# Kernel tuning notes

Measured on AMD Instinct MI355X. Metric: run time of the kernel, lower is better.

Reference implementation:

```python
import jax, jax.numpy as jnp
import numpy as np

NEG_INF = -1e9  # matches torch masked_fill value of -1000000000.0


def setup_inputs() -> dict:
    key = jax.random.key(0)
    k1, k2, k3, k4 = jax.random.split(key, 4)
    B, H, S, D = 4, 16, 2048, 128
    query = jax.random.normal(k1, (B, H, S, D), dtype=jnp.float32)
    key_t = jax.random.normal(k2, (B, H, S, D), dtype=jnp.float32)
    value = jax.random.normal(k3, (B, H, S, D), dtype=jnp.float32)
    mask = jax.random.randint(k4, (B, 1, 1, S), 0, 2, dtype=jnp.int32)
    return {"query": query, "key": key_t, "value": value, "mask": mask, "dropout": 0}


def reference(query, key, value, mask, dropout):
    # scores = Q K^T / sqrt(d_k)   [B,H,S,S]
    d_k = query.shape[-1]
    scores = jnp.einsum("bhqd,bhkd->bhqk", query, key) / jnp.sqrt(jnp.asarray(d_k, query.dtype))
    # masked_fill_(mask == 0, -1e9); mask broadcasts [B,1,1,S] -> [B,H,S,S]
    scores = jnp.where(mask == 0, jnp.asarray(NEG_INF, scores.dtype), scores)
    # dropout == 0 -> identity (deterministic reference / eval mode)
    attn = jax.nn.softmax(scores, axis=-1)
    return jnp.einsum("bhqk,bhkd->bhqd", attn, value)
```

## Files before the change

### kernel.cpp

```cpp
#include <hip/hip_runtime.h>
#include <hip/hip_bf16.h>

#define S_LEN 2048
#define D_DIM 128
#define QBLK 256
#define KVBLK 32
#define NT (S_LEN / KVBLK)
#define KCHUNK 8192
#define VCHUNK 8192
#define PRE_BYTES ((size_t)64 * NT * (KCHUNK + VCHUNK))

typedef __attribute__((ext_vector_type(8))) short short8v;
typedef __attribute__((ext_vector_type(16))) float f32x16;

static __device__ __forceinline__ unsigned f2bf2(float lo, float hi) {
    float2 f2; f2.x = lo; f2.y = hi;
    __hip_bfloat162 h2 = __float22bfloat162_rn(f2);
    unsigned r;
    __builtin_memcpy(&r, &h2, 4);
    return r;
}

static __device__ __forceinline__ void plswap(unsigned& a, unsigned& b) {
    auto r = __builtin_amdgcn_permlane32_swap(a, b, false, false);
    a = r[0]; b = r[1];
}
static __device__ __forceinline__ float plswap_sum(float x) {
    unsigned a = __float_as_uint(x), b = a;
    plswap(a, b);
    return __uint_as_float(a) + __uint_as_float(b);
}

static __device__ __forceinline__ void gload16(const void* g, void* l) {
    __builtin_amdgcn_global_load_lds(
        (const __attribute__((address_space(1))) unsigned int*)g,
        (__attribute__((address_space(3))) unsigned int*)l,
        16, 0, 0);
}

static __device__ __forceinline__ void stage8k(const unsigned char* g, unsigned char* l,
                                               int wv, int lane) {
#pragma unroll
    for (int i = 0; i < 2; ++i) {
        const int off = (wv * 2 + i) * 1024;
        gload16(g + off + lane * 16, l + off);
    }
}

#define VTS 133

__global__ __launch_bounds__(256) void preconv(
    const float* __restrict__ Kp, const float* __restrict__ Vp,
    unsigned short* __restrict__ Ko, unsigned short* __restrict__ Vo)
{
    __shared__ float vt[64 * VTS];
    const int tid = threadIdx.x;
    const int blk = blockIdx.x;
    const size_t gbase = (size_t)(blk >> 5) * S_LEN * D_DIM + (size_t)(blk & 31) * 64 * D_DIM;

#pragma unroll
    for (int i = 0; i < 8; ++i) {
        int idx = (tid + 256 * i) * 4;
        int row = idx >> 7, col = idx & 127;
        float4 v4 = *(const float4*)(Vp + gbase + idx);
        float* d = &vt[row * VTS + col];
        d[0] = v4.x; d[1] = v4.y; d[2] = v4.z; d[3] = v4.w;
    }

    unsigned short* kout = Ko + (size_t)blk * 8192;
#pragma unroll
    for (int i = 0; i < 4; ++i) {
        int o = tid + 256 * i;
        int row = o >> 4, bs = o & 15;
        int b = (bs & 8) | ((bs ^ row) & 7);
        const float* gp = Kp + gbase + row * D_DIM + 8 * b;
        float4 x = *(const float4*)gp;
        float4 y = *(const float4*)(gp + 4);
        uint4 w;
        w.x = f2bf2(x.x, x.y); w.y = f2bf2(x.z, x.w);
        w.z = f2bf2(y.x, y.y); w.w = f2bf2(y.z, y.w);
        *(uint4*)(kout + o * 8) = w;
    }
    __syncthreads();

    unsigned short* vout = Vo + (size_t)blk * 8192;
#pragma unroll
    for (int i = 0; i < 4; ++i) {
        int u = tid + 256 * i;
        int ch = u >> 9, r = u & 511;
        int d = r >> 2, bs = r & 3;
        int b = bs ^ ((d >> 1) & 3);
        const float* c0 = &vt[(ch * 32 + 8 * b) * VTS + d];
        uint4 w;
        w.x = f2bf2(c0[0 * VTS], c0[1 * VTS]);
        w.y = f2bf2(c0[2 * VTS], c0[3 * VTS]);
        w.z = f2bf2(c0[4 * VTS], c0[5 * VTS]);
        w.w = f2bf2(c0[6 * VTS], c0[7 * VTS]);
        *(uint4*)(vout + u * 8) = w;
    }
}

#define ASMEM (16384 + 16384 + 8192)

__global__ __launch_bounds__(256, 2) void sdpa_fwd_pre(
    const float* __restrict__ Qp, const unsigned short* __restrict__ Kpre,
    const unsigned short* __restrict__ Vpre, const int* __restrict__ Mp,
    float* __restrict__ Op)
{
    extern __shared__ unsigned char smem[];
    unsigned char* KbB = smem;
    unsigned char* VbB = smem + 16384;
    float* blds = (float*)(smem + 32768);

    const int tid  = threadIdx.x;
    const int lane = tid & 63;
    const int wv   = tid >> 6;
    const int h    = lane >> 5;
    const int c31  = lane & 31;
    const int hrx  = h ^ (c31 & 7);
    const int vsx  = (c31 >> 1) & 3;
    const int lbid = ((blockIdx.x & 7) << 6) | (blockIdx.x >> 3);
    const int bh   = lbid >> 3;
    const int q0   = (lbid & 7) * QBLK;
    const int bb   = bh >> 4;
    const size_t base = (size_t)bh * S_LEN * D_DIM;
    const unsigned char* Kg = (const unsigned char*)Kpre + (size_t)bh * (NT * KCHUNK);
    const unsigned char* Vg = (const unsigned char*)Vpre + (size_t)bh * (NT * VCHUNK);

    constexpr float SC   = 0.08838834764831845f * 1.4426950408889634f;
    constexpr float NEGB = -1.4426950408889634e9f;
    constexpr float M2   = 16.0f;

    {
        const int* mp = Mp + bb * S_LEN;
#pragma unroll
        for (int i = 0; i < S_LEN / 256; ++i)
            blds[tid + 256 * i] = mp[tid + 256 * i] ? -M2 : NEGB;
    }

    short8v qf0[8], qf1[8];
#pragma unroll
    for (int g = 0; g < 2; ++g) {
        const float* qrp = Qp + base + (size_t)(q0 + 64 * wv + 32 * g + c31) * D_DIM;
#pragma unroll
        for (int kk = 0; kk < 8; ++kk) {
            float4 x = *(const float4*)(qrp + 16 * kk + 8 * h);
            float4 y = *(const float4*)(qrp + 16 * kk + 8 * h + 4);
            uint4 w;
            w.x = f2bf2(x.x * SC, x.y * SC); w.y = f2bf2(x.z * SC, x.w * SC);
            w.z = f2bf2(y.x * SC, y.y * SC); w.w = f2bf2(y.z * SC, y.w * SC);
            if (g == 0) *(uint4*)&qf0[kk] = w; else *(uint4*)&qf1[kk] = w;
        }
    }

    stage8k(Kg, KbB, wv, lane);
    stage8k(Vg, VbB, wv, lane);
    __syncthreads();

    f32x16 acc0[4], acc1[4];
#pragma unroll
    for (int dt = 0; dt < 4; ++dt)
#pragma unroll
        for (int i = 0; i < 16; ++i) { acc0[dt][i] = 0.f; acc1[dt][i] = 0.f; }

    float lp0 = 0.f, lp1 = 0.f;
    int cur = 0;

#pragma unroll 1
    for (int t0 = 0; t0 < NT; ++t0) {
        const unsigned char* KcB = KbB + cur * KCHUNK;
        const unsigned char* VcB = VbB + cur * VCHUNK;

        if (t0 + 1 < NT) {
            stage8k(Kg + (size_t)(t0 + 1) * KCHUNK, KbB + (cur ^ 1) * KCHUNK, wv, lane);
            stage8k(Vg + (size_t)(t0 + 1) * VCHUNK, VbB + (cur ^ 1) * VCHUNK, wv, lane);
        }

        f32x16 s0, s1;
        {
            const float* bp = blds + t0 * KVBLK + 4 * h;
#pragma unroll
            for (int t4 = 0; t4 < 4; ++t4) {
                float4 b4 = *(const float4*)(bp + 8 * t4);
                s0[4 * t4 + 0] = b4.x; s0[4 * t4 + 1] = b4.y;
                s0[4 * t4 + 2] = b4.z; s0[4 * t4 + 3] = b4.w;
                s1[4 * t4 + 0] = b4.x; s1[4 * t4 + 1] = b4.y;
                s1[4 * t4 + 2] = b4.z; s1[4 * t4 + 3] = b4.w;
            }
        }

        __builtin_amdgcn_s_setprio(1);
        {
            const unsigned char* rowp = KcB + (c31 << 8);
#pragma unroll
            for (int kk = 0; kk < 8; ++kk) {
                const int bs = ((2 * kk) & 8) | (((2 * kk) & 7) ^ hrx);
                short8v kf = *(const short8v*)(rowp + (bs << 4));
                s0 = __builtin_amdgcn_mfma_f32_32x32x16_bf16(kf, qf0[kk], s0, 0, 0, 0);
                s1 = __builtin_amdgcn_mfma_f32_32x32x16_bf16(kf, qf1[kk], s1, 0, 0, 0);
            }
        }
        __builtin_amdgcn_s_setprio(0);

        unsigned w00[4], w10[4], w01[4], w11[4];
#pragma unroll
        for (int t4 = 0; t4 < 4; ++t4) {
            float e0 = __builtin_amdgcn_exp2f(s0[4 * t4 + 0]);
            float e1 = __builtin_amdgcn_exp2f(s0[4 * t4 + 1]);
            float e2 = __builtin_amdgcn_exp2f(s0[4 * t4 + 2]);
            float e3 = __builtin_amdgcn_exp2f(s0[4 * t4 + 3]);
            w00[t4] = f2bf2(e0, e1);
            w10[t4] = f2bf2(e2, e3);
            lp0 += (e0 + e1) + (e2 + e3);
            float f0 = __builtin_amdgcn_exp2f(s1[4 * t4 + 0]);
            float f1 = __builtin_amdgcn_exp2f(s1[4 * t4 + 1]);
            float f2 = __builtin_amdgcn_exp2f(s1[4 * t4 + 2]);
            float f3 = __builtin_amdgcn_exp2f(s1[4 * t4 + 3]);
            w01[t4] = f2bf2(f0, f1);
            w11[t4] = f2bf2(f2, f3);
            lp1 += (f0 + f1) + (f2 + f3);
        }

        __builtin_amdgcn_s_setprio(1);
#pragma unroll
        for (int kk = 0; kk < 2; ++kk) {
            unsigned ax0 = w00[2 * kk], bx0 = w00[2 * kk + 1];
            plswap(ax0, bx0);
            unsigned ay0 = w10[2 * kk], by0 = w10[2 * kk + 1];
            plswap(ay0, by0);
            uint4 pw0; pw0.x = ax0; pw0.y = ay0; pw0.z = bx0; pw0.w = by0;
            short8v pf0 = *(short8v*)&pw0;
            unsigned ax1 = w01[2 * kk], bx1 = w01[2 * kk + 1];
            plswap(ax1, bx1);
            unsigned ay1 = w11[2 * kk], by1 = w11[2 * kk + 1];
            plswap(ay1, by1);
            uint4 pw1; pw1.x = ax1; pw1.y = ay1; pw1.z = bx1; pw1.w = by1;
            short8v pf1 = *(short8v*)&pw1;
            const int bs = (2 * kk + h) ^ vsx;
#pragma unroll
            for (int dt = 0; dt < 4; ++dt) {
                short8v vf = *(const short8v*)(VcB + ((32 * dt + c31) << 6) + (bs << 4));
                acc0[dt] = __builtin_amdgcn_mfma_f32_32x32x16_bf16(vf, pf0, acc0[dt], 0, 0, 0);
                acc1[dt] = __builtin_amdgcn_mfma_f32_32x32x16_bf16(vf, pf1, acc1[dt], 0, 0, 0);
            }
        }
        __builtin_amdgcn_s_setprio(0);

        __syncthreads();
        cur ^= 1;
    }

    const float linv0 = 1.0f / plswap_sum(lp0);
    const float linv1 = 1.0f / plswap_sum(lp1);
    float* sw = (float*)(smem + wv * (32 * 68 * 4));
#define EPILOG(ACC, LINV, G)                                                     \
    {                                                                            \
        _Pragma("unroll")                                                        \
        for (int ph = 0; ph < 2; ++ph) {                                         \
            _Pragma("unroll")                                                    \
            for (int dp = 0; dp < 2; ++dp) {                                     \
                const int dtg = 2 * ph + dp;                                     \
                _Pragma("unroll")                                                \
                for (int r = 0; r < 16; ++r) {                                   \
                    int dloc = 32 * dp + (r & 3) + 8 * (r >> 2) + 4 * h;         \
                    sw[c31 * 68 + dloc] = ACC[dtg][r] * (LINV);                  \
                }                                                                \
            }                                                                    \
            _Pragma("unroll")                                                    \
            for (int it = 0; it < 8; ++it) {                                     \
                int f4 = lane + 64 * it;                                         \
                int qq = f4 >> 4, c4 = f4 & 15;                                  \
                float4 val = *(const float4*)&sw[qq * 68 + 4 * c4];              \
                *(float4*)(Op + base + (size_t)(q0 + 64 * wv + 32 * (G) + qq)    \
                           * D_DIM + 64 * ph + 4 * c4) = val;                    \
            }                                                                    \
        }                                                                        \
    }
    EPILOG(acc0, linv0, 0)
    EPILOG(acc1, linv1, 1)
#undef EPILOG
}

#define FBKV 64
#define FBNT (S_LEN / FBKV)
#define FBQB 128
#define KSTRIDE 136
#define VSTRIDE 72
#define KELEMS (FBKV * KSTRIDE)
#define VELEMS (D_DIM * VSTRIDE)
#define KBYTES (2 * KELEMS * 2)
#define VBYTES (2 * VELEMS * 2)
#define FBSMEM (KBYTES + VBYTES + S_LEN * 4)

struct KReg { float4 a[4][2]; };
struct VReg { float4 a[2][4]; };

static __device__ __forceinline__ void load_K(KReg& kr, const float* Kbase,
                                              int kv0, int kr0, int kc8) {
#pragma unroll
    for (int i = 0; i < 4; ++i) {
        const float* gp = Kbase + (size_t)(kv0 + kr0 + 16 * i) * D_DIM + 8 * kc8;
        kr.a[i][0] = *(const float4*)gp;
        kr.a[i][1] = *(const float4*)(gp + 4);
    }
}
static __device__ __forceinline__ void write_K(const KReg& kr, unsigned short* Kn,
                                               int kr0, int kc8) {
#pragma unroll
    for (int i = 0; i < 4; ++i) {
        uint4 w;
        w.x = f2bf2(kr.a[i][0].x, kr.a[i][0].y);
        w.y = f2bf2(kr.a[i][0].z, kr.a[i][0].w);
        w.z = f2bf2(kr.a[i][1].x, kr.a[i][1].y);
        w.w = f2bf2(kr.a[i][1].z, kr.a[i][1].w);
        *(uint4*)&Kn[(kr0 + 16 * i) * KSTRIDE + 8 * kc8] = w;
    }
}
static __device__ __forceinline__ void load_V(VReg& vr, const float* Vbase,
                                              int kv0, int vkq, int vdg) {
#pragma unroll
    for (int ii = 0; ii < 2; ++ii)
#pragma unroll
        for (int r = 0; r < 4; ++r)
            vr.a[ii][r] = *(const float4*)(Vbase + (size_t)(kv0 + 4 * vkq + 32 * ii + r) * D_DIM + 4 * vdg);
}
static __device__ __forceinline__ void write_V(const VReg& vr, unsigned short* Vn,
                                               int vkq, int vdg) {
#pragma unroll
    for (int ii = 0; ii < 2; ++ii) {
        const int kvb = 4 * vkq + 32 * ii;
        const int d0  = 4 * vdg;
        uint2 u;
        u.x = f2bf2(vr.a[ii][0].x, vr.a[ii][1].x); u.y = f2bf2(vr.a[ii][2].x, vr.a[ii][3].x);
        *(uint2*)&Vn[(d0 + 0) * VSTRIDE + kvb] = u;
        u.x = f2bf2(vr.a[ii][0].y, vr.a[ii][1].y); u.y = f2bf2(vr.a[ii][2].y, vr.a[ii][3].y);
        *(uint2*)&Vn[(d0 + 1) * VSTRIDE + kvb] = u;
        u.x = f2bf2(vr.a[ii][0].z, vr.a[ii][1].z); u.y = f2bf2(vr.a[ii][2].z, vr.a[ii][3].z);
        *(uint2*)&Vn[(d0 + 2) * VSTRIDE + kvb] = u;
        u.x = f2bf2(vr.a[ii][0].w, vr.a[ii][1].w); u.y = f2bf2(vr.a[ii][2].w, vr.a[ii][3].w);
        *(uint2*)&Vn[(d0 + 3) * VSTRIDE + kvb] = u;
    }
}

__global__ __launch_bounds__(256, 2) void sdpa_fwd_fb(
    const float* __restrict__ Qp, const float* __restrict__ Kp,
    const float* __restrict__ Vp, const int* __restrict__ Mp,
    float* __restrict__ Op)
{
    extern __shared__ unsigned char smem[];
    unsigned short* Kb   = (unsigned short*)smem;
    unsigned short* Vb   = (unsigned short*)(smem + KBYTES);
    float*          mlds = (float*)(smem + KBYTES + VBYTES);

    const int tid  = threadIdx.x;
    const int lane = tid & 63;
    const int wv   = tid >> 6;
    const int h    = lane >> 5;
    const int c31  = lane & 31;
    const int bid  = blockIdx.x;
    const int bh   = bid >> 4;
    const int q0   = (bid & 15) * FBQB;
    const int bb   = bh >> 4;
    const size_t base = (size_t)bh * S_LEN * D_DIM;

    constexpr float SC   = 0.08838834764831845f * 1.4426950408889634f;
    constexpr float NEGB = -1.4426950408889634e9f;
    constexpr float THR  = 11.541560327111708f;

    {
        const int* mp = Mp + bb * S_LEN;
#pragma unroll
        for (int i = 0; i < S_LEN / 256; ++i)
            mlds[tid + 256 * i] = mp[tid + 256 * i] ? 0.f : NEGB;
    }

    short8v qf[8];
    {
        const float* qrp = Qp + base + (size_t)(q0 + 32 * wv + c31) * D_DIM;
#pragma unroll
        for (int kk = 0; kk < 8; ++kk) {
            float4 x = *(const float4*)(qrp + 16 * kk + 8 * h);
            float4 y = *(const float4*)(qrp + 16 * kk + 8 * h + 4);
            uint4 w;
            w.x = f2bf2(x.x, x.y); w.y = f2bf2(x.z, x.w);
            w.z = f2bf2(y.x, y.y); w.w = f2bf2(y.z, y.w);
            *(uint4*)&qf[kk] = w;
        }
    }

    const int kc8 = tid & 15;
    const int kr0 = tid >> 4;
    const int vdg = tid & 31;
    const int vkq = tid >> 5;

    {
        KReg kr; VReg vr;
        load_K(kr, Kp + base, 0, kr0, kc8);
        load_V(vr, Vp + base, 0, vkq, vdg);
        write_K(kr, Kb, kr0, kc8);
        write_V(vr, Vb, vkq, vdg);
    }
    __syncthreads();

    f32x16 acc[4];
#pragma unroll
    for (int dt = 0; dt < 4; ++dt)
#pragma unroll
        for (int i = 0; i < 16; ++i) acc[dt][i] = 0.f;

    float m2 = -INFINITY;
    float lsum = 0.f;
    int cur = 0;

#pragma unroll 1
    for (int t0 = 0; t0 < FBNT; ++t0) {
        const int kv0 = t0 * FBKV;
        unsigned short* Kc = Kb + cur * KELEMS;
        unsigned short* Vc = Vb + cur * VELEMS;
        unsigned short* Kn = Kb + (cur ^ 1) * KELEMS;
        unsigned short* Vn = Vb + (cur ^ 1) * VELEMS;
        const bool pf = (t0 + 1 < FBNT);

        KReg kr; VReg vr;
        if (pf) {
            load_K(kr, Kp + base, kv0 + FBKV, kr0, kc8);
            load_V(vr, Vp + base, kv0 + FBKV, vkq, vdg);
        }

        f32x16 stc[2];
        __builtin_amdgcn_s_setprio(1);
#pragma unroll
        for (int c = 0; c < 2; ++c) {
            f32x16 s;
#pragma unroll
            for (int i = 0; i < 16; ++i) s[i] = 0.f;
#pragma unroll
            for (int kk = 0; kk < 8; ++kk) {
                short8v kf = *(const short8v*)&Kc[(32 * c + c31) * KSTRIDE + 16 * kk + 8 * h];
                s = __builtin_amdgcn_mfma_f32_32x32x16_bf16(kf, qf[kk], s, 0, 0, 0);
            }
            stc[c] = s;
        }
        __builtin_amdgcn_s_setprio(0);

        float p[2][16];
#pragma unroll
        for (int c = 0; c < 2; ++c)
#pragma unroll
            for (int t = 0; t < 4; ++t) {
                float4 b4 = *(const float4*)&mlds[kv0 + 32 * c + 8 * t + 4 * h];
                p[c][4 * t + 0] = fmaf(stc[c][4 * t + 0], SC, b4.x);
                p[c][4 * t + 1] = fmaf(stc[c][4 * t + 1], SC, b4.y);
                p[c][4 * t + 2] = fmaf(stc[c][4 * t + 2], SC, b4.z);
                p[c][4 * t + 3] = fmaf(stc[c][4 * t + 3], SC, b4.w);
            }

        float pmax = -INFINITY;
#pragma unroll
        for (int c = 0; c < 2; ++c)
#pragma unroll
            for (int r = 0; r < 16; ++r) pmax = fmaxf(pmax, p[c][r]);
        pmax = fmaxf(pmax, __shfl_xor(pmax, 32));
        if (!__all(pmax <= m2 + THR)) {
            float mnew = fmaxf(m2, pmax);
            float fr = __builtin_amdgcn_exp2f(m2 - mnew);
            m2 = mnew;
            lsum *= fr;
#pragma unroll
            for (int dt = 0; dt < 4; ++dt)
#pragma unroll
                for (int i = 0; i < 16; ++i) acc[dt][i] *= fr;
        }
        float ssum = 0.f;
#pragma unroll
        for (int c = 0; c < 2; ++c)
#pragma unroll
            for (int r = 0; r < 16; ++r) {
                float e = __builtin_amdgcn_exp2f(p[c][r] - m2);
                p[c][r] = e; ssum += e;
            }
        ssum += __shfl_xor(ssum, 32);
        lsum += ssum;

        unsigned w0[2][4], w1[2][4];
#pragma unroll
        for (int c = 0; c < 2; ++c)
#pragma unroll
            for (int t = 0; t < 4; ++t) {
                w0[c][t] = f2bf2(p[c][4 * t + 0], p[c][4 * t + 1]);
                w1[c][t] = f2bf2(p[c][4 * t + 2], p[c][4 * t + 3]);
            }

        __builtin_amdgcn_s_setprio(1);
#pragma unroll
        for (int kk = 0; kk < 4; ++kk) {
            const int t0i = (2 * kk) & 3,     c0i = (2 * kk) >> 2;
            const int t1i = (2 * kk + 1) & 3, c1i = (2 * kk + 1) >> 2;
            unsigned own0 = h ? w0[c1i][t1i] : w0[c0i][t0i];
            unsigned own1 = h ? w1[c1i][t1i] : w1[c0i][t0i];
            unsigned snd0 = h ? w0[c0i][t0i] : w0[c1i][t1i];
            unsigned snd1 = h ? w1[c0i][t0i] : w1[c1i][t1i];
            unsigned r0 = __shfl_xor(snd0, 32);
            unsigned r1 = __shfl_xor(snd1, 32);
            uint4 pw;
            pw.x = h ? r0 : own0;  pw.y = h ? r1 : own1;
            pw.z = h ? own0 : r0;  pw.w = h ? own1 : r1;
            short8v pfv = *(short8v*)&pw;
#pragma unroll
            for (int dt = 0; dt < 4; ++dt) {
                short8v vf = *(const short8v*)&Vc[(32 * dt + c31) * VSTRIDE + 16 * kk + 8 * h];
                acc[dt] = __builtin_amdgcn_mfma_f32_32x32x16_bf16(vf, pfv, acc[dt], 0, 0, 0);
            }
        }
        __builtin_amdgcn_s_setprio(0);

        if (pf) {
            write_K(kr, Kn, kr0, kc8);
            write_V(vr, Vn, vkq, vdg);
        }
        __syncthreads();
        cur ^= 1;
    }

    __syncthreads();
    const float linv = 1.0f / lsum;
    float* sw = (float*)(smem + wv * (32 * 68 * 4));
#pragma unroll
    for (int ph = 0; ph < 2; ++ph) {
#pragma unroll
        for (int dp = 0; dp < 2; ++dp) {
            const int dtg = 2 * ph + dp;
#pragma unroll
            for (int r = 0; r < 16; ++r) {
                int dloc = 32 * dp + (r & 3) + 8 * (r >> 2) + 4 * h;
                sw[c31 * 68 + dloc] = acc[dtg][r] * linv;
            }
        }
#pragma unroll
        for (int it = 0; it < 8; ++it) {
            int f4 = lane + 64 * it;
            int qq = f4 >> 4, c4 = f4 & 15;
            float4 val = *(const float4*)&sw[qq * 68 + 4 * c4];
            *(float4*)(Op + base + (size_t)(q0 + 32 * wv + qq) * D_DIM + 64 * ph + 4 * c4) = val;
        }
    }
}

extern "C" void kernel_launch(void* const* d_in, const int* in_sizes, int n_in,
                              void* d_out, int out_size, void* d_ws, size_t ws_size,
                              hipStream_t stream) {
    (void)in_sizes; (void)n_in; (void)out_size;
    const float* Q = (const float*)d_in[0];
    const float* K = (const float*)d_in[1];
    const float* V = (const float*)d_in[2];
    const int*   M = (const int*)d_in[3];
    float*       O = (float*)d_out;

    if (ws_size >= PRE_BYTES) {
        unsigned short* Kpre = (unsigned short*)d_ws;
        unsigned short* Vpre = (unsigned short*)((char*)d_ws + PRE_BYTES / 2);
        hipLaunchKernelGGL(preconv, dim3(64 * 32), dim3(256), 0, stream, K, V, Kpre, Vpre);
        hipLaunchKernelGGL(sdpa_fwd_pre, dim3(64 * (S_LEN / QBLK)), dim3(256), ASMEM, stream,
                           Q, Kpre, Vpre, M, O);
    } else {
        hipLaunchKernelGGL(sdpa_fwd_fb, dim3(1024), dim3(256), FBSMEM, stream, Q, K, V, M, O);
    }
}
```

Baseline: 201.6 us.

## Software-pipeline QK^T one tile ahead of softmax and PV

Restructures the main loop so the QK^T MFMA for tile t+1 is issued after the PV MFMAs of tile t, with K staged two tiles ahead and V one tile ahead. A prologue computes the first score tile before the loop. This is meant to let the exp and convert work overlap with independent MFMA chains and to hide the LDS latency of K fragments. In exchange it adds a live score register set across iterations, which may raise register pressure, and it changes the buffer indexing.

```diff
diff --git a/kernel.cpp b/kernel.cpp
--- a/kernel.cpp
+++ b/kernel.cpp
@@ -155,6 +155,7 @@
 
     stage8k(Kg, KbB, wv, lane);
     stage8k(Vg, VbB, wv, lane);
+    stage8k(Kg + KCHUNK, KbB + KCHUNK, wv, lane);
     __syncthreads();
 
     f32x16 acc0[4], acc1[4];
@@ -162,45 +163,37 @@
     for (int dt = 0; dt < 4; ++dt)
 #pragma unroll
         for (int i = 0; i < 16; ++i) { acc0[dt][i] = 0.f; acc1[dt][i] = 0.f; }
-
     float lp0 = 0.f, lp1 = 0.f;
-    int cur = 0;
+
+    f32x16 s0, s1;
+    {
+        const float* bp = blds + 4 * h;
+#pragma unroll
+        for (int t4 = 0; t4 < 4; ++t4) {
+            float4 b4 = *(const float4*)(bp + 8 * t4);
+            s0[4 * t4 + 0] = b4.x; s0[4 * t4 + 1] = b4.y;
+            s0[4 * t4 + 2] = b4.z; s0[4 * t4 + 3] = b4.w;
+            s1[4 * t4 + 0] = b4.x; s1[4 * t4 + 1] = b4.y;
+            s1[4 * t4 + 2] = b4.z; s1[4 * t4 + 3] = b4.w;
+        }
+        const unsigned char* rowp = KbB + (c31 << 8);
+#pragma unroll
+        for (int kk = 0; kk < 8; ++kk) {
+            const int bs = ((2 * kk) & 8) | (((2 * kk) & 7) ^ hrx);
+            short8v kf = *(const short8v*)(rowp + (bs << 4));
+            s0 = __builtin_amdgcn_mfma_f32_32x32x16_bf16(kf, qf0[kk], s0, 0, 0, 0);
+            s1 = __builtin_amdgcn_mfma_f32_32x32x16_bf16(kf, qf1[kk], s1, 0, 0, 0);
+        }
+    }
+    __syncthreads();
 
 #pragma unroll 1
     for (int t0 = 0; t0 < NT; ++t0) {
-        const unsigned char* KcB = KbB + cur * KCHUNK;
-        const unsigned char* VcB = VbB + cur * VCHUNK;
-
-        if (t0 + 1 < NT) {
-            stage8k(Kg + (size_t)(t0 + 1) * KCHUNK, KbB + (cur ^ 1) * KCHUNK, wv, lane);
-            stage8k(Vg + (size_t)(t0 + 1) * VCHUNK, VbB + (cur ^ 1) * VCHUNK, wv, lane);
-        }
-
-        f32x16 s0, s1;
-        {
-            const float* bp = blds + t0 * KVBLK + 4 * h;
-#pragma unroll
-            for (int t4 = 0; t4 < 4; ++t4) {
-                float4 b4 = *(const float4*)(bp + 8 * t4);
-                s0[4 * t4 + 0] = b4.x; s0[4 * t4 + 1] = b4.y;
-                s0[4 * t4 + 2] = b4.z; s0[4 * t4 + 3] = b4.w;
-                s1[4 * t4 + 0] = b4.x; s1[4 * t4 + 1] = b4.y;
-                s1[4 * t4 + 2] = b4.z; s1[4 * t4 + 3] = b4.w;
-            }
-        }
-
-        __builtin_amdgcn_s_setprio(1);
-        {
-            const unsigned char* rowp = KcB + (c31 << 8);
-#pragma unroll
-            for (int kk = 0; kk < 8; ++kk) {
-                const int bs = ((2 * kk) & 8) | (((2 * kk) & 7) ^ hrx);
-                short8v kf = *(const short8v*)(rowp + (bs << 4));
-                s0 = __builtin_amdgcn_mfma_f32_32x32x16_bf16(kf, qf0[kk], s0, 0, 0, 0);
-                s1 = __builtin_amdgcn_mfma_f32_32x32x16_bf16(kf, qf1[kk], s1, 0, 0, 0);
-            }
-        }
-        __builtin_amdgcn_s_setprio(0);
+        const unsigned char* VcB = VbB + (t0 & 1) * VCHUNK;
+        const unsigned char* KnB = KbB + ((t0 + 1) & 1) * KCHUNK;
+
+        if (t0 + 2 < NT) stage8k(Kg + (size_t)(t0 + 2) * KCHUNK, KbB + (t0 & 1) * KCHUNK, wv, lane);
+        if (t0 + 1 < NT) stage8k(Vg + (size_t)(t0 + 1) * VCHUNK, VbB + ((t0 + 1) & 1) * VCHUNK, wv, lane);
 
         unsigned w00[4], w10[4], w01[4], w11[4];
 #pragma unroll
@@ -244,10 +237,28 @@
                 acc1[dt] = __builtin_amdgcn_mfma_f32_32x32x16_bf16(vf, pf1, acc1[dt], 0, 0, 0);
             }
         }
+        if (t0 + 1 < NT) {
+            const float* bp = blds + (t0 + 1) * KVBLK + 4 * h;
+#pragma unroll
+            for (int t4 = 0; t4 < 4; ++t4) {
+                float4 b4 = *(const float4*)(bp + 8 * t4);
+                s0[4 * t4 + 0] = b4.x; s0[4 * t4 + 1] = b4.y;
+                s0[4 * t4 + 2] = b4.z; s0[4 * t4 + 3] = b4.w;
+                s1[4 * t4 + 0] = b4.x; s1[4 * t4 + 1] = b4.y;
+                s1[4 * t4 + 2] = b4.z; s1[4 * t4 + 3] = b4.w;
+            }
+            const unsigned char* rowp = KnB + (c31 << 8);
+#pragma unroll
+            for (int kk = 0; kk < 8; ++kk) {
+                const int bs = ((2 * kk) & 8) | (((2 * kk) & 7) ^ hrx);
+                short8v kf = *(const short8v*)(rowp + (bs << 4));
+                s0 = __builtin_amdgcn_mfma_f32_32x32x16_bf16(kf, qf0[kk], s0, 0, 0, 0);
+                s1 = __builtin_amdgcn_mfma_f32_32x32x16_bf16(kf, qf1[kk], s1, 0, 0, 0);
+            }
+        }
         __builtin_amdgcn_s_setprio(0);
 
         __syncthreads();
-        cur ^= 1;
     }
 
     const float linv0 = 1.0f / plswap_sum(lp0);
```

Result: slower. 248.5 us (+23.3%).
